# Performance work log

Hardware: AMD Instinct MI355X
Metric: run time of the kernel (lower is better)

Reference implementation:

```python
import jax, jax.numpy as jnp
import numpy as np

B, C_IN, H, W = 8, 112, 16, 16
D = 128            # patch_embed_dim
N_BANK = 200000
CHUNK = 1024       # query_chunk_size
NN_K = 3
TOPK_RATIO = 0.03  # reduction = 'topk_mean'


def setup_inputs() -> dict:
    key = jax.random.key(0)
    k1, k2, k3 = jax.random.split(key, 3)
    feature_map = jax.random.normal(k1, (B, C_IN, H, W), dtype=jnp.float32)
    proj_w = jax.random.normal(k2, (D, C_IN), dtype=jnp.float32) * 0.05
    memory_bank = jax.random.normal(k3, (N_BANK, D), dtype=jnp.float32)
    return {"feature_map": feature_map, "proj_w": proj_w, "memory_bank": memory_bank}


def _l2norm(x, axis=-1, eps=1e-12):
    return x / jnp.maximum(jnp.linalg.norm(x, axis=axis, keepdims=True), eps)


def reference(feature_map, proj_w, memory_bank):
    b, c, h, w = feature_map.shape
    patches = h * w
    # patch embeddings: NHWC flatten -> linear proj (no bias) -> L2 normalize
    emb = feature_map.transpose(0, 2, 3, 1).reshape(-1, c)        # [Q, C_in]
    emb = _l2norm(emb @ proj_w.T)                                  # [Q, D]
    bank = _l2norm(memory_bank)                                    # [N, D]
    bank_t = bank.T                                                # [D, N]

    q_total = emb.shape[0]
    n_chunks = q_total // CHUNK if q_total % CHUNK == 0 else -(-q_total // CHUNK)
    pad = n_chunks * CHUNK - q_total
    emb_p = jnp.pad(emb, ((0, pad), (0, 0)))
    chunks = emb_p.reshape(n_chunks, CHUNK, -1)

    def chunk_fn(q):                                               # q: [CHUNK, D]
        sims = q @ bank_t                                          # [CHUNK, N]
        best_sim, _ = jax.lax.top_k(sims, NN_K)                    # [CHUNK, k]
        dist = jnp.sqrt(jnp.maximum(2.0 - 2.0 * best_sim, 0.0))
        return dist.mean(axis=1)                                   # [CHUNK]

    patch_d = jax.lax.map(chunk_fn, chunks).reshape(-1)[:q_total]
    patch_d = patch_d.reshape(b, patches)                          # [B, P]

    # topk_mean reduction over patches
    k = min(patches, max(1, int(np.ceil(patches * TOPK_RATIO))))
    top_vals, _ = jax.lax.top_k(patch_d, k)
    return top_vals.mean(axis=1)                                   # [B]
```

## Files before the change

### kernel.cpp

```cpp
#include <hip/hip_runtime.h>
#include <stdint.h>

#define N_BANK 200000
#define N_PAD  201600
#define NQ     2048
#define DIMD   128
#define C_IN   112
#define NCHUNK 63
#define CHUNK_COLS 3200
#define NSTEP  25
#define NCE    126
#define NC3    378

typedef short v8s __attribute__((ext_vector_type(8)));
typedef float v4f __attribute__((ext_vector_type(4)));

typedef const __attribute__((address_space(1))) uint32_t* gp1_t;
typedef __attribute__((address_space(3))) uint32_t* lp3_t;

__device__ __forceinline__ void async16(const void* g, void* l) {
  __builtin_amdgcn_global_load_lds((gp1_t)g, (lp3_t)l, 16, 0, 0);
}

__device__ __forceinline__ unsigned short f2bf(float f) {
  uint32_t u = __float_as_uint(f);
  u += 0x7fff + ((u >> 16) & 1);
  return (unsigned short)(u >> 16);
}

__device__ __forceinline__ void insert3(float& m1, float& m2, float& m3, float v) {
  m3 = __builtin_amdgcn_fmed3f(m2, m3, v);
  m2 = __builtin_amdgcn_fmed3f(m1, m2, v);
  m1 = fmaxf(m1, v);
}

__global__ void emb_kernel(const float* __restrict__ fm, const float* __restrict__ pw,
                           unsigned short* __restrict__ embB) {
  int q = blockIdx.x;
  int b = q >> 8, p = q & 255;
  int tid = threadIdx.x;
  __shared__ float x[C_IN];
  __shared__ float wsum[2];
  if (tid < C_IN) x[tid] = fm[(b * C_IN + tid) * 256 + p];
  __syncthreads();
  const float* row = pw + tid * C_IN;
  float dot = 0.f;
#pragma unroll
  for (int c = 0; c < C_IN; ++c) dot = fmaf(x[c], row[c], dot);
  float s = dot * dot;
#pragma unroll
  for (int off = 32; off; off >>= 1) s += __shfl_xor(s, off);
  int lane = tid & 63, wv = tid >> 6;
  if (lane == 0) wsum[wv] = s;
  __syncthreads();
  float ss = wsum[0] + wsum[1];
  float scale = 1.f / fmaxf(sqrtf(ss), 1e-12f);
  embB[q * DIMD + tid] = f2bf(dot * scale);
}

__global__ void bank_kernel(const float* __restrict__ bank, unsigned short* __restrict__ bankB) {
  int tid = threadIdx.x;
  int wv = tid >> 6, lane = tid & 63;
  int r = blockIdx.x * 4 + wv;
  if (r >= N_PAD) return;
  uint32_t* out = (uint32_t*)bankB;
  if (r < N_BANK) {
    float2 v = ((const float2*)bank)[r * 64 + lane];
    float s = v.x * v.x + v.y * v.y;
#pragma unroll
    for (int off = 32; off; off >>= 1) s += __shfl_xor(s, off);
    float scale = 1.f / fmaxf(sqrtf(s), 1e-12f);
    uint32_t lo = f2bf(v.x * scale);
    uint32_t hi = f2bf(v.y * scale);
    out[r * 64 + lane] = lo | (hi << 16);
  } else {
    out[r * 64 + lane] = 0u;
  }
}

__global__ __launch_bounds__(256, 2)
void sim_top3_kernel(const unsigned short* __restrict__ embB,
                     const unsigned short* __restrict__ bankB,
                     float* __restrict__ partial) {
  int mt = blockIdx.x;
  int chunk = blockIdx.y;
  int q0 = mt * 128;
  int tid = threadIdx.x;
  int wv = tid >> 6, lane = tid & 63;
  int wr = wv >> 1, wc = wv & 1;
  int g = lane >> 4, c0 = lane & 15;

  __shared__ __align__(16) unsigned char lds[32768];

  {
    const char* gbase = (const char*)embB + q0 * 256;
#pragma unroll
    for (int i = 0; i < 8; ++i) {
      int off = (wv * 8 + i) * 1024 + lane * 16;
      async16(gbase + off, lds + off);
    }
  }
  __syncthreads();

  v8s a[4][4];
#pragma unroll
  for (int fm = 0; fm < 4; ++fm)
#pragma unroll
    for (int k = 0; k < 4; ++k) {
      int row = wr * 64 + fm * 16 + c0;
      a[fm][k] = *(const v8s*)(lds + row * 256 + k * 64 + g * 16);
    }

  float m1[16], m2[16], m3[16];
#pragma unroll
  for (int t = 0; t < 16; ++t) { m1[t] = -1e30f; m2[t] = -1e30f; m3[t] = -1e30f; }

  const char* bbase = (const char*)bankB + (size_t)chunk * CHUNK_COLS * 256;
  for (int s = 0; s < NSTEP; ++s) {
    __syncthreads();
#pragma unroll
    for (int i = 0; i < 8; ++i) {
      int off = (wv * 8 + i) * 1024 + lane * 16;
      async16(bbase + (size_t)s * 128 * 256 + off, lds + off);
    }
    __syncthreads();

#pragma unroll
    for (int fn = 0; fn < 4; ++fn) {
      v8s bf[4];
      int col = wc * 64 + fn * 16 + c0;
#pragma unroll
      for (int k = 0; k < 4; ++k)
        bf[k] = *(const v8s*)(lds + col * 256 + k * 64 + g * 16);
#pragma unroll
      for (int fm = 0; fm < 4; ++fm) {
        v4f acc = {0.f, 0.f, 0.f, 0.f};
#pragma unroll
        for (int k = 0; k < 4; ++k)
          acc = __builtin_amdgcn_mfma_f32_16x16x32_bf16(a[fm][k], bf[k], acc, 0, 0, 0);
#pragma unroll
        for (int j = 0; j < 4; ++j)
          insert3(m1[fm * 4 + j], m2[fm * 4 + j], m3[fm * 4 + j], acc[j]);
      }
    }
  }

#pragma unroll
  for (int mask = 1; mask < 16; mask <<= 1) {
#pragma unroll
    for (int t = 0; t < 16; ++t) {
      float b1 = __shfl_xor(m1[t], mask);
      float b2 = __shfl_xor(m2[t], mask);
      float b3 = __shfl_xor(m3[t], mask);
      insert3(m1[t], m2[t], m3[t], b1);
      insert3(m1[t], m2[t], m3[t], b2);
      insert3(m1[t], m2[t], m3[t], b3);
    }
  }

  if (c0 == 0) {
    int ce = chunk * 2 + wc;
#pragma unroll
    for (int t = 0; t < 16; ++t) {
      int q = q0 + wr * 64 + (t >> 2) * 16 + g * 4 + (t & 3);
      partial[(ce * 3 + 0) * NQ + q] = m1[t];
      partial[(ce * 3 + 1) * NQ + q] = m2[t];
      partial[(ce * 3 + 2) * NQ + q] = m3[t];
    }
  }
}

__global__ void merge_kernel(const float* __restrict__ partial, float* __restrict__ out) {
  int b = blockIdx.x;
  int tid = threadIdx.x;
  int q = b * 256 + tid;
  float m1 = -1e30f, m2 = -1e30f, m3 = -1e30f;
  for (int c = 0; c < NC3; ++c) insert3(m1, m2, m3, partial[c * NQ + q]);
  float d1 = sqrtf(fmaxf(2.f - 2.f * m1, 0.f));
  float d2 = sqrtf(fmaxf(2.f - 2.f * m2, 0.f));
  float d3 = sqrtf(fmaxf(2.f - 2.f * m3, 0.f));
  float pd = (d1 + d2 + d3) * (1.f / 3.f);

  __shared__ float vals[256];
  __shared__ float rv[256];
  __shared__ int ri[256];
  vals[tid] = pd;
  __syncthreads();
  float sum = 0.f;
  for (int iter = 0; iter < 8; ++iter) {
    rv[tid] = vals[tid]; ri[tid] = tid;
    __syncthreads();
    for (int s = 128; s > 0; s >>= 1) {
      if (tid < s && rv[tid + s] > rv[tid]) { rv[tid] = rv[tid + s]; ri[tid] = ri[tid + s]; }
      __syncthreads();
    }
    sum += rv[0];
    if (tid == 0) vals[ri[0]] = -1e30f;
    __syncthreads();
  }
  if (tid == 0) out[b] = sum * (1.f / 8.f);
}

extern "C" void kernel_launch(void* const* d_in, const int* in_sizes, int n_in,
                              void* d_out, int out_size, void* d_ws, size_t ws_size,
                              hipStream_t stream) {
  const float* fm   = (const float*)d_in[0];
  const float* pw   = (const float*)d_in[1];
  const float* bank = (const float*)d_in[2];
  float* out = (float*)d_out;

  char* ws = (char*)d_ws;
  unsigned short* bankB = (unsigned short*)ws;
  unsigned short* embB  = (unsigned short*)(ws + 51609600);
  float* partial        = (float*)(ws + 51609600 + 524288);

  emb_kernel<<<NQ, 128, 0, stream>>>(fm, pw, embB);
  bank_kernel<<<N_PAD / 4, 256, 0, stream>>>(bank, bankB);
  sim_top3_kernel<<<dim3(16, NCHUNK), 256, 0, stream>>>(embB, bankB, partial);
  merge_kernel<<<8, 256, 0, stream>>>(partial, out);
}
```

Measured before the change: 346.8 us.

## Swizzle bf16 embedding/bank layout for LDS reads and parallelize top-3 merge

The emb and bank conversion kernels now write each 128-dim bf16 row with 16-byte segments XOR-swizzled by row index, and the MFMA kernel reads LDS with the matching XOR so the strided fragment loads avoid bank conflicts. The partial top-3 buffer is transposed to query-major. The single 8-block merge is split into a wave-per-query merge across many blocks plus a small top-k reduction kernel. This adds one kernel launch and a workspace buffer, and depends on the swizzle staying consistent between producers and consumer.

```diff
diff --git a/kernel.cpp b/kernel.cpp
--- a/kernel.cpp
+++ b/kernel.cpp
@@ -55,7 +55,9 @@
   __syncthreads();
   float ss = wsum[0] + wsum[1];
   float scale = 1.f / fmaxf(sqrtf(ss), 1e-12f);
-  embB[q * DIMD + tid] = f2bf(dot * scale);
+  int j = tid >> 3, pos = tid & 7;
+  int sw = j ^ (q & 15);
+  embB[q * DIMD + sw * 8 + pos] = f2bf(dot * scale);
 }
 
 __global__ void bank_kernel(const float* __restrict__ bank, unsigned short* __restrict__ bankB) {
@@ -64,6 +66,8 @@
   int r = blockIdx.x * 4 + wv;
   if (r >= N_PAD) return;
   uint32_t* out = (uint32_t*)bankB;
+  int j = lane >> 2, w = lane & 3;
+  int sdw = ((j ^ (r & 15)) << 2) | w;
   if (r < N_BANK) {
     float2 v = ((const float2*)bank)[r * 64 + lane];
     float s = v.x * v.x + v.y * v.y;
@@ -72,9 +76,9 @@
     float scale = 1.f / fmaxf(sqrtf(s), 1e-12f);
     uint32_t lo = f2bf(v.x * scale);
     uint32_t hi = f2bf(v.y * scale);
-    out[r * 64 + lane] = lo | (hi << 16);
+    out[r * 64 + sdw] = lo | (hi << 16);
   } else {
-    out[r * 64 + lane] = 0u;
+    out[r * 64 + sdw] = 0u;
   }
 }
 
@@ -108,7 +112,7 @@
 #pragma unroll
     for (int k = 0; k < 4; ++k) {
       int row = wr * 64 + fm * 16 + c0;
-      a[fm][k] = *(const v8s*)(lds + row * 256 + k * 64 + g * 16);
+      a[fm][k] = *(const v8s*)(lds + row * 256 + (((k * 4 + g) ^ c0) << 4));
     }
 
   float m1[16], m2[16], m3[16];
@@ -131,7 +135,7 @@
       int col = wc * 64 + fn * 16 + c0;
 #pragma unroll
       for (int k = 0; k < 4; ++k)
-        bf[k] = *(const v8s*)(lds + col * 256 + k * 64 + g * 16);
+        bf[k] = *(const v8s*)(lds + col * 256 + (((k * 4 + g) ^ c0) << 4));
 #pragma unroll
       for (int fm = 0; fm < 4; ++fm) {
         v4f acc = {0.f, 0.f, 0.f, 0.f};
@@ -163,28 +167,44 @@
 #pragma unroll
     for (int t = 0; t < 16; ++t) {
       int q = q0 + wr * 64 + (t >> 2) * 16 + g * 4 + (t & 3);
-      partial[(ce * 3 + 0) * NQ + q] = m1[t];
-      partial[(ce * 3 + 1) * NQ + q] = m2[t];
-      partial[(ce * 3 + 2) * NQ + q] = m3[t];
-    }
-  }
-}
-
-__global__ void merge_kernel(const float* __restrict__ partial, float* __restrict__ out) {
+      float* dst = partial + (size_t)q * NC3 + ce * 3;
+      dst[0] = m1[t];
+      dst[1] = m2[t];
+      dst[2] = m3[t];
+    }
+  }
+}
+
+__global__ void merge1_kernel(const float* __restrict__ partial, float* __restrict__ pd) {
+  int q = (blockIdx.x * blockDim.x + threadIdx.x) >> 6;
+  int lane = threadIdx.x & 63;
+  const float* src = partial + (size_t)q * NC3;
+  float m1 = -1e30f, m2 = -1e30f, m3 = -1e30f;
+  for (int c = lane; c < NC3; c += 64) insert3(m1, m2, m3, src[c]);
+#pragma unroll
+  for (int mask = 32; mask; mask >>= 1) {
+    float b1 = __shfl_xor(m1, mask);
+    float b2 = __shfl_xor(m2, mask);
+    float b3 = __shfl_xor(m3, mask);
+    insert3(m1, m2, m3, b1);
+    insert3(m1, m2, m3, b2);
+    insert3(m1, m2, m3, b3);
+  }
+  if (lane == 0) {
+    float d1 = sqrtf(fmaxf(2.f - 2.f * m1, 0.f));
+    float d2 = sqrtf(fmaxf(2.f - 2.f * m2, 0.f));
+    float d3 = sqrtf(fmaxf(2.f - 2.f * m3, 0.f));
+    pd[q] = (d1 + d2 + d3) * (1.f / 3.f);
+  }
+}
+
+__global__ void merge2_kernel(const float* __restrict__ pd, float* __restrict__ out) {
   int b = blockIdx.x;
   int tid = threadIdx.x;
-  int q = b * 256 + tid;
-  float m1 = -1e30f, m2 = -1e30f, m3 = -1e30f;
-  for (int c = 0; c < NC3; ++c) insert3(m1, m2, m3, partial[c * NQ + q]);
-  float d1 = sqrtf(fmaxf(2.f - 2.f * m1, 0.f));
-  float d2 = sqrtf(fmaxf(2.f - 2.f * m2, 0.f));
-  float d3 = sqrtf(fmaxf(2.f - 2.f * m3, 0.f));
-  float pd = (d1 + d2 + d3) * (1.f / 3.f);
-
   __shared__ float vals[256];
   __shared__ float rv[256];
   __shared__ int ri[256];
-  vals[tid] = pd;
+  vals[tid] = pd[b * 256 + tid];
   __syncthreads();
   float sum = 0.f;
   for (int iter = 0; iter < 8; ++iter) {
@@ -213,9 +233,11 @@
   unsigned short* bankB = (unsigned short*)ws;
   unsigned short* embB  = (unsigned short*)(ws + 51609600);
   float* partial        = (float*)(ws + 51609600 + 524288);
+  float* pd             = (float*)(ws + 51609600 + 524288 + 3096576);
 
   emb_kernel<<<NQ, 128, 0, stream>>>(fm, pw, embB);
   bank_kernel<<<N_PAD / 4, 256, 0, stream>>>(bank, bankB);
   sim_top3_kernel<<<dim3(16, NCHUNK), 256, 0, stream>>>(embB, bankB, partial);
-  merge_kernel<<<8, 256, 0, stream>>>(partial, out);
-}
+  merge1_kernel<<<NQ / 4, 256, 0, stream>>>(partial, pd);
+  merge2_kernel<<<8, 256, 0, stream>>>(pd, out);
+}
```

Result: faster. 309.3 us (-10.8%).
